# Kernel optimization log

Hardware: AMD Instinct MI355X
Metric: run time of the kernel (lower is better)

Reference implementation:

```python
import jax, jax.numpy as jnp
import numpy as np

N_NODES = 50000
N_EDGES = 800000
N_GRAPHS = 1000
D_NODE = 92
D_EDGE = 41
D_HID = 128
D_OUT = 1


def _glorot(key, shape):
    fan_in, fan_out = shape[1], shape[0]
    lim = jnp.sqrt(6.0 / (fan_in + fan_out))
    return jax.random.uniform(key, shape, jnp.float32, -lim, lim)


def setup_inputs() -> dict:
    key = jax.random.key(0)
    ks = jax.random.split(key, 16)
    x = jax.random.normal(ks[0], (N_NODES, D_NODE), jnp.float32)
    edge_index = jax.random.randint(ks[1], (2, N_EDGES), 0, N_NODES, jnp.int64)
    edge_attr = jax.random.uniform(ks[2], (N_EDGES, D_EDGE), jnp.float32)
    batch = jnp.sort(jax.random.randint(ks[3], (N_NODES,), 0, N_GRAPHS, jnp.int64))
    z_in = 2 * D_HID + D_EDGE  # CGConv concat dim
    return {
        "x": x, "edge_index": edge_index, "edge_attr": edge_attr, "batch": batch,
        "W_node": _glorot(ks[4], (D_HID, D_NODE)), "b_node": jnp.zeros((D_HID,), jnp.float32),
        "Wf1": _glorot(ks[5], (D_HID, z_in)), "bf1": jnp.zeros((D_HID,), jnp.float32),
        "Ws1": _glorot(ks[6], (D_HID, z_in)), "bs1": jnp.zeros((D_HID,), jnp.float32),
        "Wf2": _glorot(ks[7], (D_HID, z_in)), "bf2": jnp.zeros((D_HID,), jnp.float32),
        "Ws2": _glorot(ks[8], (D_HID, z_in)), "bs2": jnp.zeros((D_HID,), jnp.float32),
        "W1": _glorot(ks[9], (D_HID, D_HID)), "b1": jnp.zeros((D_HID,), jnp.float32),
        "W2": _glorot(ks[10], (D_OUT, D_HID)), "b2": jnp.zeros((D_OUT,), jnp.float32),
    }


def _cgconv(h, src, dst, edge_attr, Wf, bf, Ws, bs):
    # PyG CGConv: z_ij = [x_i, x_j, e_ij]; msg = sigmoid(lin_f(z)) * softplus(lin_s(z))
    # aggr='add' at target i; residual: out = x + aggr
    z = jnp.concatenate([h[dst], h[src], edge_attr], axis=1)  # [E, 2*D_HID + D_EDGE]
    msg = jax.nn.sigmoid(z @ Wf.T + bf) * jax.nn.softplus(z @ Ws.T + bs)  # [E, D_HID]
    agg = jax.ops.segment_sum(msg, dst, num_segments=N_NODES)
    return h + agg


def reference(x, edge_index, edge_attr, batch,
              W_node, b_node, Wf1, bf1, Ws1, bs1, Wf2, bf2, Ws2, bs2,
              W1, b1, W2, b2):
    src, dst = edge_index[0], edge_index[1]  # message flows j(src) -> i(dst)
    h = jax.nn.leaky_relu(x @ W_node.T + b_node)
    h = jax.nn.leaky_relu(_cgconv(h, src, dst, edge_attr, Wf1, bf1, Ws1, bs1))
    atom_embs = jax.nn.leaky_relu(_cgconv(h, src, dst, edge_attr, Wf2, bf2, Ws2, bs2))
    pooled = jax.ops.segment_sum(atom_embs, batch, num_segments=N_GRAPHS)  # [G, D_HID]
    norm = jnp.maximum(jnp.linalg.norm(pooled, axis=1, keepdims=True), 1e-12)
    g = pooled / norm
    g = jax.nn.leaky_relu(g @ W1.T + b1)
    out = g @ W2.T + b2
    return (out, atom_embs)
```

## Files before the change

kernel.cpp:

```cpp
#include <hip/hip_runtime.h>
#include <math.h>

#define NN 50000
#define NE 800000
#define NG 1000
#define DN 92
#define DE 41
#define DH 128

typedef float f32x4 __attribute__((ext_vector_type(4)));
typedef short s16x8 __attribute__((ext_vector_type(8)));

#define OFF_A     ((size_t)0)
#define OFF_ABF   ((size_t)6400000)
#define OFF_PI    ((size_t)9600000)
#define OFF_PJ    ((size_t)16000000)
#define OFF_WCATB ((size_t)22400000)
#define OFF_WTE   ((size_t)22465536)
#define OFF_POOL  ((size_t)22481920)
#define OFF_CNT   ((size_t)22609920)
#define OFF_CUR   ((size_t)22659920)
#define OFF_SE    ((size_t)22709920)
#define OFF_SDST  ((size_t)24309920)

__device__ __forceinline__ float leaky(float x) { return x > 0.f ? x : 0.01f * x; }
__device__ __forceinline__ ushort f2bf(float x) {
    uint u = __float_as_uint(x);
    return (ushort)((u + 0x7fffu + ((u >> 16) & 1u)) >> 16);
}
__device__ __forceinline__ float bflo(uint u) { return __uint_as_float(u << 16); }
__device__ __forceinline__ float bfhi(uint u) { return __uint_as_float(u & 0xffff0000u); }

__global__ __launch_bounds__(128) void k_node_embed(const float* __restrict__ x,
        const float* __restrict__ Wn, const float* __restrict__ bn,
        float* __restrict__ A, ushort* __restrict__ Abf) {
    __shared__ __align__(16) float xs[16 * DN];
    const int n0 = blockIdx.x * 16;
    const int t = threadIdx.x;
    const float4* xg = (const float4*)(x + (size_t)n0 * DN);
    float4* xs4 = (float4*)xs;
    for (int i = t; i < 16 * DN / 4; i += 128) xs4[i] = xg[i];
    __syncthreads();
    const int o = t;
    float acc[16];
#pragma unroll
    for (int n = 0; n < 16; n++) acc[n] = 0.f;
    const float4* Wr = (const float4*)(Wn + (size_t)o * DN);
    for (int kk = 0; kk < DN / 4; kk++) {
        float4 w = Wr[kk];
#pragma unroll
        for (int n = 0; n < 16; n++) {
            float4 a = ((const float4*)(xs + n * DN))[kk];
            acc[n] = fmaf(w.x, a.x, acc[n]);
            acc[n] = fmaf(w.y, a.y, acc[n]);
            acc[n] = fmaf(w.z, a.z, acc[n]);
            acc[n] = fmaf(w.w, a.w, acc[n]);
        }
    }
    float b = bn[o];
#pragma unroll
    for (int n = 0; n < 16; n++) {
        float v = leaky(acc[n] + b);
        A[(size_t)(n0 + n) * DH + o] = v;
        Abf[(size_t)(n0 + n) * DH + o] = f2bf(v);
    }
}

__global__ __launch_bounds__(128) void k_pack_wcatb(const float* __restrict__ Wf1,
        const float* __restrict__ Ws1, const float* __restrict__ Wf2,
        const float* __restrict__ Ws2, ushort* __restrict__ Wcatb) {
    int b = blockIdx.x;
    int l = b >> 9, row = b & 511;
    int cb = row >> 7, o = row & 127;
    const float* src;
    if (l == 0) src = (cb < 2) ? Wf1 : Ws1;
    else        src = (cb < 2) ? Wf2 : Ws2;
    int koff = (cb & 1) * 128;
    Wcatb[(size_t)b * 128 + threadIdx.x] = f2bf(src[(size_t)o * 297 + koff + threadIdx.x]);
}

__global__ __launch_bounds__(64) void k_pack_wte(const float* __restrict__ Wf1,
        const float* __restrict__ Ws1, const float* __restrict__ Wf2,
        const float* __restrict__ Ws2, ushort* __restrict__ Wte) {
    int n = blockIdx.x, layer = blockIdx.y, k = threadIdx.x;
    int c = n >> 1, g = n & 1;
    const float* W = layer ? (g ? Ws2 : Wf2) : (g ? Ws1 : Wf1);
    float v = (k < DE) ? W[(size_t)c * 297 + 256 + k] : 0.f;
    Wte[((size_t)(layer * 256 + n)) * 64 + k] = f2bf(v);
}

__global__ __launch_bounds__(256) void k_hist(const int* __restrict__ ei,
        int* __restrict__ cnt) {
    int e = blockIdx.x * 256 + threadIdx.x;
    atomicAdd(&cnt[ei[NE + e]], 1);
}

__global__ __launch_bounds__(1024) void k_scan(const int* __restrict__ cnt,
        int* __restrict__ cur) {
    __shared__ int part[1024];
    const int t = threadIdx.x;
    const int lo = t * 49, hi = min(lo + 49, NN);
    int s = 0;
    for (int i = lo; i < hi; i++) s += cnt[i];
    part[t] = s;
    __syncthreads();
    for (int off = 1; off < 1024; off <<= 1) {
        int u = (t >= off) ? part[t - off] : 0;
        __syncthreads();
        part[t] += u;
        __syncthreads();
    }
    int run = part[t] - s;
    for (int i = lo; i < hi; i++) { int c = cnt[i]; cur[i] = run; run += c; }
}

__global__ __launch_bounds__(256) void k_scatter(const int* __restrict__ ei,
        int* __restrict__ cur, uint2* __restrict__ se, int* __restrict__ sdst) {
    int e = blockIdx.x * 256 + threadIdx.x;
    int src = ei[e], dst = ei[NE + e];
    int pos = atomicAdd(&cur[dst], 1);
    se[pos] = make_uint2((uint)src, (uint)e);
    sdst[pos] = dst;
}

__global__ __launch_bounds__(256) void k_gemm_P2(const ushort* __restrict__ Abf,
        const ushort* __restrict__ Wcatb, const float* __restrict__ bf,
        const float* __restrict__ bs, ushort* __restrict__ Pi,
        ushort* __restrict__ Pj) {
    __shared__ ushort Alds[32 * 136];
    __shared__ ushort OTi[32 * 264];
    __shared__ ushort OTj[32 * 264];
    const int n0 = blockIdx.x * 32;
    const int t = threadIdx.x;
    const int cb = t >> 6, l = t & 63, m16 = l & 15, g = l >> 4;

    const uint4* Ag = (const uint4*)Abf;
#pragma unroll
    for (int p = 0; p < 2; p++) {
        int row = (t >> 4) + p * 16;
        int node = n0 + row;
        uint4 v = make_uint4(0u, 0u, 0u, 0u);
        if (node < NN) v = Ag[(size_t)node * 16 + (t & 15)];
        *(uint4*)(Alds + row * 136 + (t & 15) * 8) = v;
    }
    __syncthreads();

    const ushort* Bw = Wcatb + (size_t)cb * 128 * 128;
    f32x4 acc[2][8];
#pragma unroll
    for (int mt = 0; mt < 2; mt++)
#pragma unroll
        for (int nt = 0; nt < 8; nt++) acc[mt][nt] = (f32x4){0.f, 0.f, 0.f, 0.f};

    for (int ks = 0; ks < 4; ks++) {
        s16x8 bfr[8];
#pragma unroll
        for (int nt = 0; nt < 8; nt++)
            bfr[nt] = *(const s16x8*)(Bw + ((size_t)(nt * 16 + m16)) * 128 + ks * 32 + g * 8);
        s16x8 afr[2];
#pragma unroll
        for (int mt = 0; mt < 2; mt++)
            afr[mt] = *(const s16x8*)(Alds + (mt * 16 + m16) * 136 + ks * 32 + g * 8);
#pragma unroll
        for (int mt = 0; mt < 2; mt++)
#pragma unroll
            for (int nt = 0; nt < 8; nt++)
                acc[mt][nt] = __builtin_amdgcn_mfma_f32_16x16x32_bf16(
                    afr[mt], bfr[nt], acc[mt][nt], 0, 0, 0);
    }

    float bias[8];
#pragma unroll
    for (int nt = 0; nt < 8; nt++) bias[nt] = 0.f;
    if (cb == 0) {
#pragma unroll
        for (int nt = 0; nt < 8; nt++) bias[nt] = bf[nt * 16 + m16];
    } else if (cb == 2) {
#pragma unroll
        for (int nt = 0; nt < 8; nt++) bias[nt] = bs[nt * 16 + m16];
    }
    ushort* OT = (cb & 1) ? OTj : OTi;
    const int sel = cb >> 1;
#pragma unroll
    for (int mt = 0; mt < 2; mt++)
#pragma unroll
        for (int nt = 0; nt < 8; nt++)
#pragma unroll
            for (int r = 0; r < 4; r++)
                OT[(mt * 16 + g * 4 + r) * 264 + (nt * 16 + m16) * 2 + sel] =
                    f2bf(acc[mt][nt][r] + bias[nt]);
    __syncthreads();
#pragma unroll
    for (int p = 0; p < 4; p++) {
        int idx = t + p * 256;
        int row = idx >> 5, col8 = idx & 31;
        int node = n0 + row;
        if (node < NN) {
            *(uint4*)(Pi + (size_t)node * 256 + col8 * 8) = *(const uint4*)(OTi + row * 264 + col8 * 8);
            *(uint4*)(Pj + (size_t)node * 256 + col8 * 8) = *(const uint4*)(OTj + row * 264 + col8 * 8);
        }
    }
}

__global__ __launch_bounds__(256) void k_edge(const ushort* __restrict__ Pi,
        const ushort* __restrict__ Pj, const uint2* __restrict__ se,
        const int* __restrict__ sdst, const float* __restrict__ ea,
        const ushort* __restrict__ Wte, float* __restrict__ A) {
    __shared__ ushort Elds[32 * 264];
    const int t = threadIdx.x, w = t >> 6, l = t & 63;
    const int e0 = blockIdx.x * 32;
    const int m16 = l & 15, g = l >> 4;

    s16x8 bt[4][2];
#pragma unroll
    for (int nt = 0; nt < 4; nt++)
#pragma unroll
        for (int ks = 0; ks < 2; ks++)
            bt[nt][ks] = *(const s16x8*)(Wte + ((size_t)(w * 64 + nt * 16 + m16)) * 64 + ks * 32 + g * 8);

    s16x8 at[2][2];
#pragma unroll
    for (int mt = 0; mt < 2; mt++) {
        uint2 s2 = se[e0 + mt * 16 + m16];
        const float* row = ea + (size_t)s2.y * DE;
        float v[8];
#pragma unroll
        for (int j = 0; j < 8; j++) v[j] = row[g * 8 + j];
        s16x8 a0;
#pragma unroll
        for (int j = 0; j < 8; j++) a0[j] = (short)f2bf(v[j]);
        at[mt][0] = a0;
        float v1[8];
#pragma unroll
        for (int j = 0; j < 8; j++) v1[j] = 0.f;
        if (g == 0) {
#pragma unroll
            for (int j = 0; j < 8; j++) v1[j] = row[32 + j];
        } else if (g == 1) {
            v1[0] = row[40];
        }
        s16x8 a1;
#pragma unroll
        for (int j = 0; j < 8; j++) a1[j] = (short)f2bf(v1[j]);
        at[mt][1] = a1;
    }

    f32x4 acc[2][4];
#pragma unroll
    for (int mt = 0; mt < 2; mt++)
#pragma unroll
        for (int nt = 0; nt < 4; nt++)
            acc[mt][nt] = (f32x4){0.f, 0.f, 0.f, 0.f};
#pragma unroll
    for (int ks = 0; ks < 2; ks++)
#pragma unroll
        for (int mt = 0; mt < 2; mt++)
#pragma unroll
            for (int nt = 0; nt < 4; nt++)
                acc[mt][nt] = __builtin_amdgcn_mfma_f32_16x16x32_bf16(
                    at[mt][ks], bt[nt][ks], acc[mt][nt], 0, 0, 0);

#pragma unroll
    for (int mt = 0; mt < 2; mt++)
#pragma unroll
        for (int nt = 0; nt < 4; nt++)
#pragma unroll
            for (int r = 0; r < 4; r++)
                Elds[(mt * 16 + g * 4 + r) * 264 + w * 64 + nt * 16 + m16] =
                    f2bf(acc[mt][nt][r]);
    __syncthreads();

    const uint* PiU = (const uint*)Pi;
    const uint* PjU = (const uint*)Pj;
    const uint* ElU = (const uint*)Elds;
    const int base = e0 + w * 8;
    int dsts[8];
    float msg[8][2];
#pragma unroll
    for (int i = 0; i < 8; i++) {
        const int src = __builtin_amdgcn_readfirstlane((int)se[base + i].x);
        const int dst = __builtin_amdgcn_readfirstlane(sdst[base + i]);
        dsts[i] = dst;
        uint pj0 = PjU[(size_t)src * 128 + l];
        uint pj1 = PjU[(size_t)src * 128 + 64 + l];
        uint pi0 = PiU[(size_t)dst * 128 + l];
        uint pi1 = PiU[(size_t)dst * 128 + 64 + l];
        uint ev0 = ElU[(w * 8 + i) * 132 + l];
        uint ev1 = ElU[(w * 8 + i) * 132 + 64 + l];
        float f0 = bflo(pi0) + bflo(pj0) + bflo(ev0);
        float s0 = bfhi(pi0) + bfhi(pj0) + bfhi(ev0);
        float f1 = bflo(pi1) + bflo(pj1) + bflo(ev1);
        float s1 = bfhi(pi1) + bfhi(pj1) + bfhi(ev1);
        float sg0 = 1.f / (1.f + __expf(-f0));
        float sg1 = 1.f / (1.f + __expf(-f1));
        float sp0 = fmaxf(s0, 0.f) + __logf(1.f + __expf(-fabsf(s0)));
        float sp1 = fmaxf(s1, 0.f) + __logf(1.f + __expf(-fabsf(s1)));
        msg[i][0] = sg0 * sp0;
        msg[i][1] = sg1 * sp1;
    }
    float a0 = msg[0][0], a1 = msg[0][1];
#pragma unroll
    for (int i = 1; i < 8; i++) {
        if (dsts[i] == dsts[i - 1]) {
            a0 += msg[i][0]; a1 += msg[i][1];
        } else {
            atomicAdd(A + (size_t)dsts[i - 1] * DH + l, a0);
            atomicAdd(A + (size_t)dsts[i - 1] * DH + 64 + l, a1);
            a0 = msg[i][0]; a1 = msg[i][1];
        }
    }
    atomicAdd(A + (size_t)dsts[7] * DH + l, a0);
    atomicAdd(A + (size_t)dsts[7] * DH + 64 + l, a1);
}

__global__ __launch_bounds__(256) void k_act(float* __restrict__ A,
        ushort* __restrict__ Abf) {
    int i = blockIdx.x * 256 + threadIdx.x;
    float4* A4 = (float4*)A;
    float4 v = A4[i];
    v.x = leaky(v.x); v.y = leaky(v.y); v.z = leaky(v.z); v.w = leaky(v.w);
    A4[i] = v;
    ((uint2*)Abf)[i] = make_uint2((uint)f2bf(v.x) | ((uint)f2bf(v.y) << 16),
                                  (uint)f2bf(v.z) | ((uint)f2bf(v.w) << 16));
}

__global__ __launch_bounds__(256) void k_finalize(const float* __restrict__ A,
        const int* __restrict__ batch, float* __restrict__ embs,
        float* __restrict__ pooled) {
    int idx = blockIdx.x * 256 + threadIdx.x;
    int n = idx >> 7, o = idx & 127;
    float v = leaky(A[idx]);
    embs[idx] = v;
    atomicAdd(pooled + (size_t)batch[n] * DH + o, v);
}

__global__ __launch_bounds__(128) void k_head(const float* __restrict__ pooled,
        const float* __restrict__ W1, const float* __restrict__ b1,
        const float* __restrict__ W2, const float* __restrict__ b2,
        float* __restrict__ out) {
    __shared__ __align__(16) float gl[128];
    __shared__ float red[2];
    const int g = blockIdx.x, o = threadIdx.x;
    const int l = o & 63, wid = o >> 6;
    float p = pooled[(size_t)g * DH + o];
    float v = p * p;
#pragma unroll
    for (int off = 32; off >= 1; off >>= 1) v += __shfl_xor(v, off);
    if (l == 0) red[wid] = v;
    __syncthreads();
    float nrm = fmaxf(sqrtf(red[0] + red[1]), 1e-12f);
    float gv = p / nrm;
    gl[o] = gv;
    __syncthreads();
    float gm = b1[o];
    const float4* Wr = (const float4*)(W1 + (size_t)o * DH);
    const float4* gl4 = (const float4*)gl;
    for (int kk = 0; kk < 32; kk++) {
        float4 w = Wr[kk]; float4 a = gl4[kk];
        gm = fmaf(w.x, a.x, gm); gm = fmaf(w.y, a.y, gm);
        gm = fmaf(w.z, a.z, gm); gm = fmaf(w.w, a.w, gm);
    }
    gm = leaky(gm);
    float c = gm * W2[o];
#pragma unroll
    for (int off = 32; off >= 1; off >>= 1) c += __shfl_xor(c, off);
    __syncthreads();
    if (l == 0) red[wid] = c;
    __syncthreads();
    if (o == 0) out[g] = red[0] + red[1] + b2[0];
}

extern "C" void kernel_launch(void* const* d_in, const int* in_sizes, int n_in,
                              void* d_out, int out_size, void* d_ws, size_t ws_size,
                              hipStream_t stream) {
    const float* x    = (const float*)d_in[0];
    const int*   ei   = (const int*)d_in[1];
    const float* ea   = (const float*)d_in[2];
    const int*   batch= (const int*)d_in[3];
    const float* Wn   = (const float*)d_in[4];
    const float* bn   = (const float*)d_in[5];
    const float* Wf1  = (const float*)d_in[6];
    const float* bf1  = (const float*)d_in[7];
    const float* Ws1  = (const float*)d_in[8];
    const float* bs1  = (const float*)d_in[9];
    const float* Wf2  = (const float*)d_in[10];
    const float* bf2  = (const float*)d_in[11];
    const float* Ws2  = (const float*)d_in[12];
    const float* bs2  = (const float*)d_in[13];
    const float* W1   = (const float*)d_in[14];
    const float* b1   = (const float*)d_in[15];
    const float* W2   = (const float*)d_in[16];
    const float* b2   = (const float*)d_in[17];

    float* ws      = (float*)d_ws;
    float*  A      = ws + OFF_A;
    ushort* Abf    = (ushort*)(ws + OFF_ABF);
    ushort* Pi     = (ushort*)(ws + OFF_PI);
    ushort* Pj     = (ushort*)(ws + OFF_PJ);
    ushort* Wcatb  = (ushort*)(ws + OFF_WCATB);
    ushort* Wte    = (ushort*)(ws + OFF_WTE);
    float*  pooled = ws + OFF_POOL;
    int*    cnt    = (int*)(ws + OFF_CNT);
    int*    cur    = (int*)(ws + OFF_CUR);
    uint2*  se     = (uint2*)(ws + OFF_SE);
    int*    sdst   = (int*)(ws + OFF_SDST);
    float* out     = (float*)d_out;
    float* embs    = out + NG;

    hipMemsetAsync(pooled, 0, (size_t)NG * DH * sizeof(float), stream);
    hipMemsetAsync(cnt, 0, (size_t)NN * sizeof(int), stream);
    k_pack_wcatb<<<1024, 128, 0, stream>>>(Wf1, Ws1, Wf2, Ws2, Wcatb);
    k_pack_wte<<<dim3(256, 2), 64, 0, stream>>>(Wf1, Ws1, Wf2, Ws2, Wte);
    k_node_embed<<<NN / 16, 128, 0, stream>>>(x, Wn, bn, A, Abf);

    k_hist<<<NE / 256, 256, 0, stream>>>(ei, cnt);
    k_scan<<<1, 1024, 0, stream>>>(cnt, cur);
    k_scatter<<<NE / 256, 256, 0, stream>>>(ei, cur, se, sdst);

    k_gemm_P2<<<(NN + 31) / 32, 256, 0, stream>>>(Abf, Wcatb, bf1, bs1, Pi, Pj);
    k_edge<<<NE / 32, 256, 0, stream>>>(Pi, Pj, se, sdst, ea, Wte, A);
    k_act<<<(NN * DH / 4) / 256, 256, 0, stream>>>(A, Abf);

    k_gemm_P2<<<(NN + 31) / 32, 256, 0, stream>>>(Abf, Wcatb + (size_t)512 * 128, bf2, bs2, Pi, Pj);
    k_edge<<<NE / 32, 256, 0, stream>>>(Pi, Pj, se, sdst, ea, Wte + (size_t)256 * 64, A);

    k_finalize<<<NN * DH / 256, 256, 0, stream>>>(A, batch, embs, pooled);
    k_head<<<NG, 128, 0, stream>>>(pooled, W1, b1, W2, b2, out);
}
```

Baseline: 735.0 us.

## Restructure edge kernel: per-wave 16-edge MFMA with fp32 edge term in registers

The edge kernel now has each wave handle 16 edges and compute the full 256-wide edge-attribute projection with MFMA. The projection stays in fp32 registers, replacing the bf16 round-trip through shared memory and the block-wide barrier. The gate/shift projection layouts (Pi/Pj and the packed edge weights) change from interleaved to split halves so the accumulator fragments line up with 4-wide Pi/Pj loads. Gated messages go through per-wave LDS for the segmented atomic reduction, and bf16 packing uses the hardware convert instruction. Register pressure rises with 16 accumulators, and the atomic run-length now spans 16 edges instead of 8.

```diff
diff --git a/kernel.cpp b/kernel.cpp
--- a/kernel.cpp
+++ b/kernel.cpp
@@ -31,6 +31,20 @@
 __device__ __forceinline__ float bflo(uint u) { return __uint_as_float(u << 16); }
 __device__ __forceinline__ float bfhi(uint u) { return __uint_as_float(u & 0xffff0000u); }
 
+__device__ __forceinline__ float gate(float f, float s) {
+    float sg = 1.f / (1.f + __expf(-f));
+    float sp = fmaxf(s, 0.f) + __logf(1.f + __expf(-fabsf(s)));
+    return sg * sp;
+}
+
+__device__ __forceinline__ s16x8 pack8(const float* v) {
+    union { uint u[4]; s16x8 s; } r;
+#pragma unroll
+    for (int p = 0; p < 4; p++)
+        asm("v_cvt_pk_bf16_f32 %0, %1, %2" : "=v"(r.u[p]) : "v"(v[2 * p]), "v"(v[2 * p + 1]));
+    return r.s;
+}
+
 __global__ __launch_bounds__(128) void k_node_embed(const float* __restrict__ x,
         const float* __restrict__ Wn, const float* __restrict__ bn,
         float* __restrict__ A, ushort* __restrict__ Abf) {
@@ -81,12 +95,12 @@
 
 __global__ __launch_bounds__(64) void k_pack_wte(const float* __restrict__ Wf1,
         const float* __restrict__ Ws1, const float* __restrict__ Wf2,
-        const float* __restrict__ Ws2, ushort* __restrict__ Wte) {
+        const float* __restrict__ Ws2, ushort* __restrict__ Wte2) {
     int n = blockIdx.x, layer = blockIdx.y, k = threadIdx.x;
-    int c = n >> 1, g = n & 1;
-    const float* W = layer ? (g ? Ws2 : Wf2) : (g ? Ws1 : Wf1);
+    int c = n & 127, gsel = n >> 7;
+    const float* W = layer ? (gsel ? Ws2 : Wf2) : (gsel ? Ws1 : Wf1);
     float v = (k < DE) ? W[(size_t)c * 297 + 256 + k] : 0.f;
-    Wte[((size_t)(layer * 256 + n)) * 64 + k] = f2bf(v);
+    Wte2[((size_t)(layer * 256 + n)) * 64 + k] = f2bf(v);
 }
 
 __global__ __launch_bounds__(256) void k_hist(const int* __restrict__ ei,
@@ -180,14 +194,14 @@
         for (int nt = 0; nt < 8; nt++) bias[nt] = bs[nt * 16 + m16];
     }
     ushort* OT = (cb & 1) ? OTj : OTi;
-    const int sel = cb >> 1;
+    const int half = (cb >> 1) * 128;
 #pragma unroll
     for (int mt = 0; mt < 2; mt++)
 #pragma unroll
         for (int nt = 0; nt < 8; nt++)
 #pragma unroll
             for (int r = 0; r < 4; r++)
-                OT[(mt * 16 + g * 4 + r) * 264 + (nt * 16 + m16) * 2 + sel] =
+                OT[(mt * 16 + g * 4 + r) * 264 + half + nt * 16 + m16] =
                     f2bf(acc[mt][nt][r] + bias[nt]);
     __syncthreads();
 #pragma unroll
@@ -205,112 +219,83 @@
 __global__ __launch_bounds__(256) void k_edge(const ushort* __restrict__ Pi,
         const ushort* __restrict__ Pj, const uint2* __restrict__ se,
         const int* __restrict__ sdst, const float* __restrict__ ea,
-        const ushort* __restrict__ Wte, float* __restrict__ A) {
-    __shared__ ushort Elds[32 * 264];
+        const ushort* __restrict__ Wte2, float* __restrict__ A) {
+    __shared__ float Mlds[4 * 16 * 132];
     const int t = threadIdx.x, w = t >> 6, l = t & 63;
-    const int e0 = blockIdx.x * 32;
     const int m16 = l & 15, g = l >> 4;
-
-    s16x8 bt[4][2];
-#pragma unroll
-    for (int nt = 0; nt < 4; nt++)
-#pragma unroll
-        for (int ks = 0; ks < 2; ks++)
-            bt[nt][ks] = *(const s16x8*)(Wte + ((size_t)(w * 64 + nt * 16 + m16)) * 64 + ks * 32 + g * 8);
-
-    s16x8 at[2][2];
-#pragma unroll
-    for (int mt = 0; mt < 2; mt++) {
-        uint2 s2 = se[e0 + mt * 16 + m16];
-        const float* row = ea + (size_t)s2.y * DE;
-        float v[8];
-#pragma unroll
-        for (int j = 0; j < 8; j++) v[j] = row[g * 8 + j];
-        s16x8 a0;
-#pragma unroll
-        for (int j = 0; j < 8; j++) a0[j] = (short)f2bf(v[j]);
-        at[mt][0] = a0;
-        float v1[8];
-#pragma unroll
-        for (int j = 0; j < 8; j++) v1[j] = 0.f;
-        if (g == 0) {
-#pragma unroll
-            for (int j = 0; j < 8; j++) v1[j] = row[32 + j];
-        } else if (g == 1) {
-            v1[0] = row[40];
+    const int e0 = blockIdx.x * 64 + w * 16;
+    const int es = e0 + m16;
+    const uint2 sev = se[es];
+    const int srcL = (int)sev.x;
+    const int dstL = sdst[es];
+
+    const float* row = ea + (size_t)sev.y * DE;
+    float v0[8];
+#pragma unroll
+    for (int j = 0; j < 8; j++) v0[j] = row[g * 8 + j];
+    float v1[8];
+#pragma unroll
+    for (int j = 0; j < 8; j++) v1[j] = 0.f;
+    if (g == 0) {
+#pragma unroll
+        for (int j = 0; j < 8; j++) v1[j] = row[32 + j];
+    } else if (g == 1) {
+        v1[0] = row[40];
+    }
+    s16x8 b0 = pack8(v0), b1 = pack8(v1);
+
+    f32x4 acc[16];
+#pragma unroll
+    for (int mt = 0; mt < 16; mt++) acc[mt] = (f32x4){0.f, 0.f, 0.f, 0.f};
+#pragma unroll
+    for (int mt = 0; mt < 16; mt++) {
+        s16x8 a0 = *(const s16x8*)(Wte2 + ((size_t)(mt * 16 + m16)) * 64 + g * 8);
+        s16x8 a1 = *(const s16x8*)(Wte2 + ((size_t)(mt * 16 + m16)) * 64 + 32 + g * 8);
+        acc[mt] = __builtin_amdgcn_mfma_f32_16x16x32_bf16(a0, b0, acc[mt], 0, 0, 0);
+        acc[mt] = __builtin_amdgcn_mfma_f32_16x16x32_bf16(a1, b1, acc[mt], 0, 0, 0);
+    }
+
+    float* Mw = Mlds + w * (16 * 132);
+    const ushort* PiB = Pi + (size_t)dstL * 256;
+    const ushort* PjB = Pj + (size_t)srcL * 256;
+#pragma unroll
+    for (int a = 0; a < 8; a++) {
+        uint2 fiv = *(const uint2*)(PiB + a * 16 + 4 * g);
+        uint2 siv = *(const uint2*)(PiB + 128 + a * 16 + 4 * g);
+        uint2 fjv = *(const uint2*)(PjB + a * 16 + 4 * g);
+        uint2 sjv = *(const uint2*)(PjB + 128 + a * 16 + 4 * g);
+        float4 msg;
+        float f, s;
+        f = bflo(fiv.x) + bflo(fjv.x) + acc[a][0];
+        s = bflo(siv.x) + bflo(sjv.x) + acc[a + 8][0];
+        msg.x = gate(f, s);
+        f = bfhi(fiv.x) + bfhi(fjv.x) + acc[a][1];
+        s = bfhi(siv.x) + bfhi(sjv.x) + acc[a + 8][1];
+        msg.y = gate(f, s);
+        f = bflo(fiv.y) + bflo(fjv.y) + acc[a][2];
+        s = bflo(siv.y) + bflo(sjv.y) + acc[a + 8][2];
+        msg.z = gate(f, s);
+        f = bfhi(fiv.y) + bfhi(fjv.y) + acc[a][3];
+        s = bfhi(siv.y) + bfhi(sjv.y) + acc[a + 8][3];
+        msg.w = gate(f, s);
+        *(float4*)(Mw + m16 * 132 + a * 16 + 4 * g) = msg;
+    }
+
+    float c0 = Mw[l], c1 = Mw[64 + l];
+    int dprev = __builtin_amdgcn_readlane(dstL, 0);
+#pragma unroll
+    for (int i = 1; i < 16; i++) {
+        int d = __builtin_amdgcn_readlane(dstL, i);
+        float m0 = Mw[i * 132 + l], m1 = Mw[i * 132 + 64 + l];
+        if (d == dprev) { c0 += m0; c1 += m1; }
+        else {
+            atomicAdd(A + (size_t)dprev * DH + l, c0);
+            atomicAdd(A + (size_t)dprev * DH + 64 + l, c1);
+            c0 = m0; c1 = m1; dprev = d;
         }
-        s16x8 a1;
-#pragma unroll
-        for (int j = 0; j < 8; j++) a1[j] = (short)f2bf(v1[j]);
-        at[mt][1] = a1;
-    }
-
-    f32x4 acc[2][4];
-#pragma unroll
-    for (int mt = 0; mt < 2; mt++)
-#pragma unroll
-        for (int nt = 0; nt < 4; nt++)
-            acc[mt][nt] = (f32x4){0.f, 0.f, 0.f, 0.f};
-#pragma unroll
-    for (int ks = 0; ks < 2; ks++)
-#pragma unroll
-        for (int mt = 0; mt < 2; mt++)
-#pragma unroll
-            for (int nt = 0; nt < 4; nt++)
-                acc[mt][nt] = __builtin_amdgcn_mfma_f32_16x16x32_bf16(
-                    at[mt][ks], bt[nt][ks], acc[mt][nt], 0, 0, 0);
-
-#pragma unroll
-    for (int mt = 0; mt < 2; mt++)
-#pragma unroll
-        for (int nt = 0; nt < 4; nt++)
-#pragma unroll
-            for (int r = 0; r < 4; r++)
-                Elds[(mt * 16 + g * 4 + r) * 264 + w * 64 + nt * 16 + m16] =
-                    f2bf(acc[mt][nt][r]);
-    __syncthreads();
-
-    const uint* PiU = (const uint*)Pi;
-    const uint* PjU = (const uint*)Pj;
-    const uint* ElU = (const uint*)Elds;
-    const int base = e0 + w * 8;
-    int dsts[8];
-    float msg[8][2];
-#pragma unroll
-    for (int i = 0; i < 8; i++) {
-        const int src = __builtin_amdgcn_readfirstlane((int)se[base + i].x);
-        const int dst = __builtin_amdgcn_readfirstlane(sdst[base + i]);
-        dsts[i] = dst;
-        uint pj0 = PjU[(size_t)src * 128 + l];
-        uint pj1 = PjU[(size_t)src * 128 + 64 + l];
-        uint pi0 = PiU[(size_t)dst * 128 + l];
-        uint pi1 = PiU[(size_t)dst * 128 + 64 + l];
-        uint ev0 = ElU[(w * 8 + i) * 132 + l];
-        uint ev1 = ElU[(w * 8 + i) * 132 + 64 + l];
-        float f0 = bflo(pi0) + bflo(pj0) + bflo(ev0);
-        float s0 = bfhi(pi0) + bfhi(pj0) + bfhi(ev0);
-        float f1 = bflo(pi1) + bflo(pj1) + bflo(ev1);
-        float s1 = bfhi(pi1) + bfhi(pj1) + bfhi(ev1);
-        float sg0 = 1.f / (1.f + __expf(-f0));
-        float sg1 = 1.f / (1.f + __expf(-f1));
-        float sp0 = fmaxf(s0, 0.f) + __logf(1.f + __expf(-fabsf(s0)));
-        float sp1 = fmaxf(s1, 0.f) + __logf(1.f + __expf(-fabsf(s1)));
-        msg[i][0] = sg0 * sp0;
-        msg[i][1] = sg1 * sp1;
-    }
-    float a0 = msg[0][0], a1 = msg[0][1];
-#pragma unroll
-    for (int i = 1; i < 8; i++) {
-        if (dsts[i] == dsts[i - 1]) {
-            a0 += msg[i][0]; a1 += msg[i][1];
-        } else {
-            atomicAdd(A + (size_t)dsts[i - 1] * DH + l, a0);
-            atomicAdd(A + (size_t)dsts[i - 1] * DH + 64 + l, a1);
-            a0 = msg[i][0]; a1 = msg[i][1];
-        }
-    }
-    atomicAdd(A + (size_t)dsts[7] * DH + l, a0);
-    atomicAdd(A + (size_t)dsts[7] * DH + 64 + l, a1);
+    }
+    atomicAdd(A + (size_t)dprev * DH + l, c0);
+    atomicAdd(A + (size_t)dprev * DH + 64 + l, c1);
 }
 
 __global__ __launch_bounds__(256) void k_act(float* __restrict__ A,
@@ -398,7 +383,7 @@
     ushort* Pi     = (ushort*)(ws + OFF_PI);
     ushort* Pj     = (ushort*)(ws + OFF_PJ);
     ushort* Wcatb  = (ushort*)(ws + OFF_WCATB);
-    ushort* Wte    = (ushort*)(ws + OFF_WTE);
+    ushort* Wte2   = (ushort*)(ws + OFF_WTE);
     float*  pooled = ws + OFF_POOL;
     int*    cnt    = (int*)(ws + OFF_CNT);
     int*    cur    = (int*)(ws + OFF_CUR);
@@ -410,7 +395,7 @@
     hipMemsetAsync(pooled, 0, (size_t)NG * DH * sizeof(float), stream);
     hipMemsetAsync(cnt, 0, (size_t)NN * sizeof(int), stream);
     k_pack_wcatb<<<1024, 128, 0, stream>>>(Wf1, Ws1, Wf2, Ws2, Wcatb);
-    k_pack_wte<<<dim3(256, 2), 64, 0, stream>>>(Wf1, Ws1, Wf2, Ws2, Wte);
+    k_pack_wte<<<dim3(256, 2), 64, 0, stream>>>(Wf1, Ws1, Wf2, Ws2, Wte2);
     k_node_embed<<<NN / 16, 128, 0, stream>>>(x, Wn, bn, A, Abf);
 
     k_hist<<<NE / 256, 256, 0, stream>>>(ei, cnt);
@@ -418,11 +403,11 @@
     k_scatter<<<NE / 256, 256, 0, stream>>>(ei, cur, se, sdst);
 
     k_gemm_P2<<<(NN + 31) / 32, 256, 0, stream>>>(Abf, Wcatb, bf1, bs1, Pi, Pj);
-    k_edge<<<NE / 32, 256, 0, stream>>>(Pi, Pj, se, sdst, ea, Wte, A);
+    k_edge<<<NE / 64, 256, 0, stream>>>(Pi, Pj, se, sdst, ea, Wte2, A);
     k_act<<<(NN * DH / 4) / 256, 256, 0, stream>>>(A, Abf);
 
     k_gemm_P2<<<(NN + 31) / 32, 256, 0, stream>>>(Abf, Wcatb + (size_t)512 * 128, bf2, bs2, Pi, Pj);
-    k_edge<<<NE / 32, 256, 0, stream>>>(Pi, Pj, se, sdst, ea, Wte + (size_t)256 * 64, A);
+    k_edge<<<NE / 64, 256, 0, stream>>>(Pi, Pj, se, sdst, ea, Wte2 + (size_t)256 * 64, A);
 
     k_finalize<<<NN * DH / 256, 256, 0, stream>>>(A, batch, embs, pooled);
     k_head<<<NG, 128, 0, stream>>>(pooled, W1, b1, W2, b2, out);
```

Result: slower. 926.4 us (+26.0%).
